# Optimization experiments

Hardware: AMD Instinct MI355X
Metric: run time of the kernel (lower is better)

## Reference

```python
import jax, jax.numpy as jnp
import numpy as np

LN_EPS = 1e-5  # torch nn.LayerNorm default


def _ln(x, g, b):
    m = x.mean(-1, keepdims=True)
    v = ((x - m) ** 2).mean(-1, keepdims=True)
    return (x - m) / jnp.sqrt(v + LN_EPS) * g + b


def setup_inputs() -> dict:
    key = jax.random.key(0)
    ks = jax.random.split(key, 4)
    N, S, D, C = 64, 512, 512, 1024
    return {
        "sequence": jax.random.normal(ks[0], (N, S, D), dtype=jnp.float32),
        "input_mask": jnp.ones((N, S), dtype=jnp.float32),
        "START": jnp.zeros((D,), dtype=jnp.float32),
        "W_init": (jax.random.normal(ks[1], (D, D), dtype=jnp.float32) / np.sqrt(D)).astype(jnp.float32),
        "b_init": jnp.zeros((D,), dtype=jnp.float32),
        "W1": (jax.random.normal(ks[2], (2 * D, C), dtype=jnp.float32) / np.sqrt(2 * D)).astype(jnp.float32),
        "b1": jnp.zeros((C,), dtype=jnp.float32),
        "W2": (jax.random.normal(ks[3], (C, 4 * D), dtype=jnp.float32) / np.sqrt(C)).astype(jnp.float32),
        "b2": jnp.zeros((4 * D,), dtype=jnp.float32),
        "ln_g": jnp.ones((D,), dtype=jnp.float32),
        "ln_b": jnp.zeros((D,), dtype=jnp.float32),
    }


def reference(sequence, input_mask, START, W_init, b_init, W1, b1, W2, b2, ln_g, ln_b):
    N, S, D = sequence.shape
    mask = input_mask[..., None]                      # [N,S,1]
    seq = sequence * mask
    # initial transform: LN(Linear(x)), then re-mask
    seq = _ln(seq @ W_init + b_init, ln_g, ln_b) * mask

    ht0 = jnp.broadcast_to(START, (N, D))

    def step(carry, xs):
        ht, gs = carry
        x, m = xs                                     # x: [N,D], m: [N,1]
        cat = jnp.concatenate([ht, x], axis=-1)       # [N,2D]
        inter = jax.nn.gelu(cat @ W1 + b1)            # [N,C] (dropout: eval mode)
        contents = (inter @ W2 + b2).reshape(N, 4, D)
        gates = jax.nn.sigmoid(contents[:, :3])       # f1, f2, i
        f1, f2, i = gates[:, 0], gates[:, 1], gates[:, 2]
        parent = contents[:, 3]
        ht_new = _ln(f1 * ht + f2 * x + i * parent, ln_g, ln_b)
        gs_new = m * ht_new + (1.0 - m) * gs
        return (ht_new, gs_new), ht_new

    xs = (jnp.swapaxes(seq, 0, 1), jnp.swapaxes(mask, 0, 1))  # time-major
    (ht, global_state), outs = jax.lax.scan(step, (ht0, ht0), xs)
    out_seq = jnp.swapaxes(outs, 0, 1) * mask         # [N,S,D]
    return out_seq, global_state
```

## Files before the change

kernel.cpp:

```cpp
#include <hip/hip_runtime.h>
#include <math.h>

#define DD 512
#define SS 512
#define NB 64
#define CC 1024
#define FF 2048
#define LN_EPS 1e-5f

__device__ __forceinline__ float sigf(float x) {
  return 1.0f / (1.0f + __expf(-x));
}
__device__ __forceinline__ float geluf(float x) {
  float u = 1.5957691216057308f * (x + 0.044715f * x * x * x);
  return x / (1.0f + __expf(-u));
}

__device__ __forceinline__ float cload(const float* p) {
  return __hip_atomic_load(p, __ATOMIC_RELAXED, __HIP_MEMORY_SCOPE_AGENT);
}
__device__ __forceinline__ unsigned cloadu(const unsigned* p) {
  return __hip_atomic_load(p, __ATOMIC_RELAXED, __HIP_MEMORY_SCOPE_AGENT);
}
__device__ __forceinline__ unsigned long long cload8(
    const unsigned long long* p) {
  return __hip_atomic_load(p, __ATOMIC_RELAXED, __HIP_MEMORY_SCOPE_AGENT);
}
__device__ __forceinline__ void cstore(float* p, float v) {
  __hip_atomic_store(p, v, __ATOMIC_RELAXED, __HIP_MEMORY_SCOPE_AGENT);
}
__device__ __forceinline__ void cstoreu(unsigned* p, unsigned v) {
  __hip_atomic_store(p, v, __ATOMIC_RELAXED, __HIP_MEMORY_SCOPE_AGENT);
}
__device__ __forceinline__ void cstore2(float* p, float a, float b) {
  float2 v = make_float2(a, b);
  unsigned long long u;
  __builtin_memcpy(&u, &v, 8);
  __hip_atomic_store((unsigned long long*)p, u, __ATOMIC_RELAXED,
                     __HIP_MEMORY_SCOPE_AGENT);
}
__device__ __forceinline__ float2 u2f2(unsigned long long u) {
  float2 f;
  __builtin_memcpy(&f, &u, 8);
  return f;
}

__device__ __forceinline__ void gbar(unsigned* __restrict__ flags,
                                     unsigned ep) {
  asm volatile("s_waitcnt vmcnt(0) lgkmcnt(0)" ::: "memory");
  __syncthreads();
  if (threadIdx.x < 64) {
    if (threadIdx.x == 0) cstoreu(&flags[blockIdx.x], ep);
    const unsigned* fp = flags + (threadIdx.x << 2);
    for (;;) {
      unsigned f0 = cloadu(fp + 0);
      unsigned f1 = cloadu(fp + 1);
      unsigned f2 = cloadu(fp + 2);
      unsigned f3 = cloadu(fp + 3);
      int ok = (f0 >= ep) & (f1 >= ep) & (f2 >= ep) & (f3 >= ep);
      if (__all(ok)) break;
      __builtin_amdgcn_s_sleep(1);
    }
  }
  __syncthreads();
}

__global__ __launch_bounds__(256) void k_gemm_init(
    const float* __restrict__ A, const float* __restrict__ mask,
    const float* __restrict__ W, const float* __restrict__ bias,
    float* __restrict__ out) {
  __shared__ float As[16][65];
  __shared__ float Bs[16][65];
  const int tid = threadIdx.x;
  const int bm = blockIdx.y * 64;
  const int bn = blockIdx.x * 64;
  const int tx = tid & 15;
  const int ty = tid >> 4;
  const int idx = tid * 4;
  const int am = idx >> 4;
  const int ak = idx & 15;
  const int bk = idx >> 6;
  const int bn2 = idx & 63;
  const float mrow = mask[bm + am];
  float acc[4][4] = {};
  for (int k0 = 0; k0 < DD; k0 += 16) {
    float4 av = *(const float4*)(A + (size_t)(bm + am) * DD + k0 + ak);
    As[ak + 0][am] = av.x * mrow;
    As[ak + 1][am] = av.y * mrow;
    As[ak + 2][am] = av.z * mrow;
    As[ak + 3][am] = av.w * mrow;
    float4 bv = *(const float4*)(W + (size_t)(k0 + bk) * DD + bn + bn2);
    Bs[bk][bn2 + 0] = bv.x;
    Bs[bk][bn2 + 1] = bv.y;
    Bs[bk][bn2 + 2] = bv.z;
    Bs[bk][bn2 + 3] = bv.w;
    __syncthreads();
#pragma unroll
    for (int kk = 0; kk < 16; ++kk) {
      float a0 = As[kk][ty * 4 + 0], a1 = As[kk][ty * 4 + 1];
      float a2 = As[kk][ty * 4 + 2], a3 = As[kk][ty * 4 + 3];
      float b0 = Bs[kk][tx * 4 + 0], b1v = Bs[kk][tx * 4 + 1];
      float b2v = Bs[kk][tx * 4 + 2], b3 = Bs[kk][tx * 4 + 3];
      acc[0][0] = fmaf(a0, b0, acc[0][0]);
      acc[0][1] = fmaf(a0, b1v, acc[0][1]);
      acc[0][2] = fmaf(a0, b2v, acc[0][2]);
      acc[0][3] = fmaf(a0, b3, acc[0][3]);
      acc[1][0] = fmaf(a1, b0, acc[1][0]);
      acc[1][1] = fmaf(a1, b1v, acc[1][1]);
      acc[1][2] = fmaf(a1, b2v, acc[1][2]);
      acc[1][3] = fmaf(a1, b3, acc[1][3]);
      acc[2][0] = fmaf(a2, b0, acc[2][0]);
      acc[2][1] = fmaf(a2, b1v, acc[2][1]);
      acc[2][2] = fmaf(a2, b2v, acc[2][2]);
      acc[2][3] = fmaf(a2, b3, acc[2][3]);
      acc[3][0] = fmaf(a3, b0, acc[3][0]);
      acc[3][1] = fmaf(a3, b1v, acc[3][1]);
      acc[3][2] = fmaf(a3, b2v, acc[3][2]);
      acc[3][3] = fmaf(a3, b3, acc[3][3]);
    }
    __syncthreads();
  }
#pragma unroll
  for (int i2 = 0; i2 < 4; ++i2) {
    int row = bm + ty * 4 + i2;
#pragma unroll
    for (int j = 0; j < 4; ++j) {
      int col = bn + tx * 4 + j;
      out[(size_t)row * DD + col] = acc[i2][j] + bias[col];
    }
  }
}

__global__ __launch_bounds__(256) void k_ln_rows(
    float* __restrict__ io, const float* __restrict__ mask,
    const float* __restrict__ g, const float* __restrict__ b) {
  const int r = blockIdx.x;
  float* row = io + (size_t)r * DD;
  const int tid = threadIdx.x;
  float x0 = row[tid], x1 = row[tid + 256];
  float s = x0 + x1, ss = x0 * x0 + x1 * x1;
#pragma unroll
  for (int off = 32; off > 0; off >>= 1) {
    s += __shfl_down(s, off, 64);
    ss += __shfl_down(ss, off, 64);
  }
  __shared__ float red[8];
  int lane = tid & 63, wv = tid >> 6;
  if (lane == 0) { red[wv] = s; red[4 + wv] = ss; }
  __syncthreads();
  s = red[0] + red[1] + red[2] + red[3];
  ss = red[4] + red[5] + red[6] + red[7];
  float mean = s * (1.0f / DD);
  float var = ss * (1.0f / DD) - mean * mean;
  float rs = rsqrtf(var + LN_EPS);
  float m = mask[r];
  row[tid] = ((x0 - mean) * rs * g[tid] + b[tid]) * m;
  row[tid + 256] = ((x1 - mean) * rs * g[tid + 256] + b[tid + 256]) * m;
}

__global__ __launch_bounds__(256) void k_xt(const float* __restrict__ seq2,
                                            float* __restrict__ xT) {
  __shared__ float tl[64][65];
  const int t = blockIdx.x;
  const int kt = blockIdx.y * 64;
  const int n = threadIdx.x >> 2;
  const int f = threadIdx.x & 3;
#pragma unroll
  for (int u = 0; u < 4; ++u) {
    int k = f * 16 + u * 4;
    float4 v = *(const float4*)(seq2 + ((size_t)n * SS + t) * DD + kt + k);
    tl[k + 0][n] = v.x;
    tl[k + 1][n] = v.y;
    tl[k + 2][n] = v.z;
    tl[k + 3][n] = v.w;
  }
  __syncthreads();
  const int k2 = threadIdx.x >> 2;
#pragma unroll
  for (int u = 0; u < 4; ++u) {
    int nn = f * 16 + u * 4;
    float4 v = make_float4(tl[k2][nn], tl[k2][nn + 1], tl[k2][nn + 2],
                           tl[k2][nn + 3]);
    *(float4*)(xT + ((size_t)t * DD + kt + k2) * 64 + nn) = v;
  }
}

__global__ __launch_bounds__(256) void k_pack1(const float* __restrict__ W1,
                                               const float* __restrict__ ln_g,
                                               float* __restrict__ W1p) {
  int i = blockIdx.x * 256 + threadIdx.x;
  int bcol = i >> 13;
  int k = (i >> 3) & 1023;
  int c = i & 7;
  float v = W1[(size_t)k * CC + (bcol << 3) + c];
  if (k < 512) v *= ln_g[k];
  W1p[i] = v;
}

__global__ __launch_bounds__(256) void k_pack2(const float* __restrict__ W2,
                                               float* __restrict__ W2p) {
  int i = blockIdx.x * 256 + threadIdx.x;
  int bcol = i >> 14;
  int k = (i >> 4) & 1023;
  int j = i & 15;
  int q = j & 3;
  int dd = j >> 2;
  W2p[i] = W2[(size_t)k * FF + q * 512 + (bcol << 2) + dd];
}

__global__ __launch_bounds__(128) void k_cols(
    const float* __restrict__ W1, const float* __restrict__ b1,
    const float* __restrict__ ln_g, const float* __restrict__ ln_b,
    const float* __restrict__ START, float* __restrict__ Qc,
    float* __restrict__ Blnc, float* __restrict__ H0c,
    unsigned* __restrict__ sync) {
  int c = blockIdx.x * 128 + threadIdx.x;
  sync[c] = 0u;
  float q = 0.f, bl = 0.f, h = 0.f;
  for (int k = 0; k < 512; ++k) {
    float wv = W1[(size_t)k * CC + c];
    q = fmaf(ln_g[k], wv, q);
    bl = fmaf(ln_b[k], wv, bl);
    h = fmaf(START[k], wv, h);
  }
  float bias = b1[c];
  Qc[c] = q;
  Blnc[c] = bl + bias;
  H0c[c] = h + bias;
}

__global__ __launch_bounds__(512, 1) void scan_kernel(
    float* __restrict__ outseq, float* __restrict__ gsout,
    const float* __restrict__ mask, const float* __restrict__ START,
    const float* __restrict__ W1p, const float* __restrict__ W2p,
    const float* __restrict__ b2, const float* __restrict__ ln_g,
    const float* __restrict__ ln_b, const float* __restrict__ Qc,
    const float* __restrict__ Blnc, const float* __restrict__ H0c,
    float* __restrict__ interT, float* __restrict__ zT,
    float* __restrict__ st_sum, float* __restrict__ st_ss,
    const float* __restrict__ xT, unsigned* __restrict__ sync,
    const int use_xt) {
  const int b = blockIdx.x;
  const int bcol = b >> 1;
  const int bhalf = b & 1;
  const int tid = threadIdx.x;
  const int w = tid >> 6;
  const int lane = tid & 63;
  unsigned ep = 0;

  __shared__ float4 pA4[8][64];
  __shared__ float4 pB4[8][64][2];
  __shared__ float W1s[8192];
  __shared__ float W2s[16384];

  {
    const float4* w1src = (const float4*)(W1p + ((size_t)bcol << 13));
    const float4* w2src = (const float4*)(W2p + ((size_t)bcol << 14));
#pragma unroll
    for (int i = 0; i < 4; ++i)
      ((float4*)W1s)[tid + 512 * i] = w1src[tid + 512 * i];
#pragma unroll
    for (int i = 0; i < 8; ++i)
      ((float4*)W2s)[tid + 512 * i] = w2src[tid + 512 * i];
  }

  const int on = (bhalf << 5) + (tid & 31);
  const int oh = tid >> 5;
  const int dbase = (bcol << 2) + (oh << 1);
  const int colbase = (bcol << 3) + (oh << 2);
  float ht0 = 0, ht1 = 0, gs0 = 0, gs1 = 0, z0 = 0, z1 = 0;
  float gg0 = 0, gg1 = 0, bb0 = 0, bb1 = 0, mn = 0, rv = 0;
  float4 Q4 = make_float4(0, 0, 0, 0), Bl4 = Q4, H04 = Q4;
  float bb2[8];
  if (tid < 64) {
    ht0 = START[dbase];
    ht1 = START[dbase + 1];
    gs0 = ht0;
    gs1 = ht1;
    gg0 = ln_g[dbase];
    gg1 = ln_g[dbase + 1];
    bb0 = ln_b[dbase];
    bb1 = ln_b[dbase + 1];
    Q4 = *(const float4*)(Qc + colbase);
    Bl4 = *(const float4*)(Blnc + colbase);
    H04 = *(const float4*)(H0c + colbase);
#pragma unroll
    for (int q = 0; q < 4; ++q) {
      bb2[q] = b2[q * 512 + dbase];
      bb2[4 + q] = b2[q * 512 + dbase + 1];
    }
  }
  __syncthreads();

  for (int t = 0; t < SS; ++t) {
    if (t > 0 && tid < 64) {
      const int par9 = ((t - 1) & 1) << 9;
      const float* sp = st_sum + par9 + (on << 3);
      const float* qp = st_ss + par9 + (on << 3);
      float s = 0.f, ss = 0.f;
#pragma unroll
      for (int i = 0; i < 8; ++i) {
        s += cload(sp + i);
        ss += cload(qp + i);
      }
      float mean = s * (1.0f / DD);
      float var = ss * (1.0f / DD) - mean * mean;
      float rsv = rsqrtf(var + LN_EPS);
      mn = mean;
      rv = rsv;
      float hn0 = (z0 - mean) * rsv * gg0 + bb0;
      float hn1 = (z1 - mean) * rsv * gg1 + bb1;
      float m = mask[on * SS + (t - 1)];
      float* op =
          outseq + (size_t)on * SS * DD + (size_t)(t - 1) * DD + dbase;
      if (use_xt) {
        *(float2*)op = make_float2(hn0 * m, hn1 * m);
      } else {
        cstore2(op, hn0 * m, hn1 * m);
      }
      gs0 = m * hn0 + (1.0f - m) * gs0;
      gs1 = m * hn1 + (1.0f - m) * gs1;
      ht0 = hn0;
      ht1 = hn1;
    }
    if (b == 0) {
      const int parz9 = (t & 1) << 9;
      cstore(st_sum + parz9 + tid, 0.f);
      cstore(st_ss + parz9 + tid, 0.f);
    }
    {
      const int h = lane >> 5;
      const int bl = lane & 31;
      float4 acc = make_float4(0.f, 0.f, 0.f, 0.f);
      if (w < 4) {
        if (t > 0) {
          const float* ap = zT + (w << 13) + (bhalf << 6) + (bl << 1);
          const float* wp = W1s + (w << 10);
          for (int c0 = 0; c0 < 64; c0 += 32) {
            unsigned long long v[32];
#pragma unroll
            for (int j = 0; j < 32; ++j)
              v[j] = cload8(
                  (const unsigned long long*)(ap + ((c0 + j) << 7)));
#pragma unroll
            for (int j = 0; j < 32; ++j) {
              float2 zv = u2f2(v[j]);
              const float* wr = wp + ((c0 + j) << 4) + (h << 2);
              acc.x = fmaf(zv.x, wr[0], acc.x);
              acc.y = fmaf(zv.x, wr[1], acc.y);
              acc.z = fmaf(zv.x, wr[2], acc.z);
              acc.w = fmaf(zv.x, wr[3], acc.w);
              acc.x = fmaf(zv.y, wr[8], acc.x);
              acc.y = fmaf(zv.y, wr[9], acc.y);
              acc.z = fmaf(zv.y, wr[10], acc.z);
              acc.w = fmaf(zv.y, wr[11], acc.w);
            }
          }
        }
      } else {
        const int kxb = (w - 4) << 7;
        const float* wp = W1s + ((512 + kxb) << 3);
        if (use_xt) {
          const float* xp =
              xT + (((size_t)t * DD + kxb) << 6) + (bhalf << 5) + bl;
          for (int c0 = 0; c0 < 128; c0 += 64) {
            float v[64];
#pragma unroll
            for (int j = 0; j < 64; ++j) v[j] = xp[(c0 + j) << 6];
#pragma unroll
            for (int j = 0; j < 64; ++j) {
              const float* wr = wp + ((c0 + j) << 3) + (h << 2);
              acc.x = fmaf(v[j], wr[0], acc.x);
              acc.y = fmaf(v[j], wr[1], acc.y);
              acc.z = fmaf(v[j], wr[2], acc.z);
              acc.w = fmaf(v[j], wr[3], acc.w);
            }
          }
        } else {
          const int n = (bhalf << 5) + bl;
          const float* op =
              outseq + (size_t)n * SS * DD + (size_t)t * DD + kxb;
          for (int c0 = 0; c0 < 128; c0 += 16) {
            float4 xv[4];
#pragma unroll
            for (int j = 0; j < 4; ++j)
              xv[j] = *(const float4*)(op + c0 + 4 * j);
#pragma unroll
            for (int j = 0; j < 16; ++j) {
              const float* wr = wp + ((c0 + j) << 3) + (h << 2);
              float x = ((const float*)xv)[j];
              acc.x = fmaf(x, wr[0], acc.x);
              acc.y = fmaf(x, wr[1], acc.y);
              acc.z = fmaf(x, wr[2], acc.z);
              acc.w = fmaf(x, wr[3], acc.w);
            }
          }
        }
      }
      pA4[w][lane] = acc;
    }
    __syncthreads();
    if (tid < 64) {
      float4 P = pA4[0][tid];
      float4 X = pA4[4][tid];
#pragma unroll
      for (int ww = 1; ww < 4; ++ww) {
        float4 p = pA4[ww][tid];
        P.x += p.x; P.y += p.y; P.z += p.z; P.w += p.w;
        float4 x4 = pA4[ww + 4][tid];
        X.x += x4.x; X.y += x4.y; X.z += x4.z; X.w += x4.w;
      }
      float4 o;
      if (t > 0) {
        float c1 = -rv * mn;
        o.x = fmaf(rv, P.x, fmaf(c1, Q4.x, Bl4.x)) + X.x;
        o.y = fmaf(rv, P.y, fmaf(c1, Q4.y, Bl4.y)) + X.y;
        o.z = fmaf(rv, P.z, fmaf(c1, Q4.z, Bl4.z)) + X.z;
        o.w = fmaf(rv, P.w, fmaf(c1, Q4.w, Bl4.w)) + X.w;
      } else {
        o.x = H04.x + X.x;
        o.y = H04.y + X.y;
        o.z = H04.z + X.z;
        o.w = H04.w + X.w;
      }
      cstore2(interT + ((colbase >> 1) << 7) + (on << 1), geluf(o.x),
              geluf(o.y));
      cstore2(interT + (((colbase >> 1) + 1) << 7) + (on << 1), geluf(o.z),
              geluf(o.w));
    }
    gbar(sync, ++ep);
    {
      const int h = lane >> 5;
      const int bl = lane & 31;
      float4 accL = make_float4(0.f, 0.f, 0.f, 0.f);
      float4 accH = make_float4(0.f, 0.f, 0.f, 0.f);
      const float* w2 = W2s + (w << 11);
      const float* ip = interT + (w << 13) + (bhalf << 6) + (bl << 1);
      for (int c0 = 0; c0 < 64; c0 += 32) {
        unsigned long long v[32];
#pragma unroll
        for (int j = 0; j < 32; ++j)
          v[j] = cload8((const unsigned long long*)(ip + ((c0 + j) << 7)));
#pragma unroll
        for (int j = 0; j < 32; ++j) {
          float2 iv = u2f2(v[j]);
          const float* wr = w2 + ((c0 + j) << 5) + (h << 3);
          accL.x = fmaf(iv.x, wr[0], accL.x);
          accL.y = fmaf(iv.x, wr[1], accL.y);
          accL.z = fmaf(iv.x, wr[2], accL.z);
          accL.w = fmaf(iv.x, wr[3], accL.w);
          accH.x = fmaf(iv.x, wr[4], accH.x);
          accH.y = fmaf(iv.x, wr[5], accH.y);
          accH.z = fmaf(iv.x, wr[6], accH.z);
          accH.w = fmaf(iv.x, wr[7], accH.w);
          accL.x = fmaf(iv.y, wr[16], accL.x);
          accL.y = fmaf(iv.y, wr[17], accL.y);
          accL.z = fmaf(iv.y, wr[18], accL.z);
          accL.w = fmaf(iv.y, wr[19], accL.w);
          accH.x = fmaf(iv.y, wr[20], accH.x);
          accH.y = fmaf(iv.y, wr[21], accH.y);
          accH.z = fmaf(iv.y, wr[22], accH.z);
          accH.w = fmaf(iv.y, wr[23], accH.w);
        }
      }
      pB4[w][lane][0] = accL;
      pB4[w][lane][1] = accH;
    }
    __syncthreads();
    if (tid < 64) {
      float4 lo = pB4[0][tid][0];
      float4 hi = pB4[0][tid][1];
#pragma unroll
      for (int ww = 1; ww < 8; ++ww) {
        float4 p = pB4[ww][tid][0];
        lo.x += p.x; lo.y += p.y; lo.z += p.z; lo.w += p.w;
        float4 q = pB4[ww][tid][1];
        hi.x += q.x; hi.y += q.y; hi.z += q.z; hi.w += q.w;
      }
      lo.x += bb2[0]; lo.y += bb2[1]; lo.z += bb2[2]; lo.w += bb2[3];
      hi.x += bb2[4]; hi.y += bb2[5]; hi.z += bb2[6]; hi.w += bb2[7];
      float x0, x1;
      if (use_xt) {
        x0 = xT[((size_t)t * DD + dbase) * 64 + on];
        x1 = xT[((size_t)t * DD + dbase + 1) * 64 + on];
      } else {
        float2 x2 = *(const float2*)(outseq + (size_t)on * SS * DD +
                                     (size_t)t * DD + dbase);
        x0 = x2.x;
        x1 = x2.y;
      }
      z0 = sigf(lo.x) * ht0 + sigf(lo.y) * x0 + sigf(lo.z) * lo.w;
      z1 = sigf(hi.x) * ht1 + sigf(hi.y) * x1 + sigf(hi.z) * hi.w;
      cstore2(zT + ((dbase >> 1) << 7) + (on << 1), z0, z1);
      const int par9 = (t & 1) << 9;
      const int slot = bcol & 7;
      atomicAdd(st_sum + par9 + (on << 3) + slot, z0 + z1);
      atomicAdd(st_ss + par9 + (on << 3) + slot, z0 * z0 + z1 * z1);
    }
    gbar(sync, ++ep);
  }
  if (tid < 64) {
    const int par9 = ((SS - 1) & 1) << 9;
    const float* sp = st_sum + par9 + (on << 3);
    const float* qp = st_ss + par9 + (on << 3);
    float s = 0.f, ss = 0.f;
#pragma unroll
    for (int i = 0; i < 8; ++i) {
      s += cload(sp + i);
      ss += cload(qp + i);
    }
    float mean = s * (1.0f / DD);
    float var = ss * (1.0f / DD) - mean * mean;
    float rsv = rsqrtf(var + LN_EPS);
    float hn0 = (z0 - mean) * rsv * gg0 + bb0;
    float hn1 = (z1 - mean) * rsv * gg1 + bb1;
    float m = mask[on * SS + (SS - 1)];
    *(float2*)(outseq + (size_t)on * SS * DD + (size_t)(SS - 1) * DD +
               dbase) = make_float2(hn0 * m, hn1 * m);
    gs0 = m * hn0 + (1.0f - m) * gs0;
    gs1 = m * hn1 + (1.0f - m) * gs1;
    *(float2*)(gsout + on * DD + dbase) = make_float2(gs0, gs1);
  }
}

extern "C" void kernel_launch(void* const* d_in, const int* in_sizes, int n_in,
                              void* d_out, int out_size, void* d_ws,
                              size_t ws_size, hipStream_t stream) {
  const float* seq = (const float*)d_in[0];
  const float* mask = (const float*)d_in[1];
  const float* START = (const float*)d_in[2];
  const float* W_init = (const float*)d_in[3];
  const float* b_init = (const float*)d_in[4];
  const float* W1 = (const float*)d_in[5];
  const float* b1 = (const float*)d_in[6];
  const float* W2 = (const float*)d_in[7];
  const float* b2 = (const float*)d_in[8];
  const float* ln_g = (const float*)d_in[9];
  const float* ln_b = (const float*)d_in[10];

  float* out = (float*)d_out;
  float* outseq = out;
  float* gsout = out + (size_t)NB * SS * DD;

  float* W1p = (float*)d_ws;
  float* W2p = W1p + 1048576;
  float* interT = W2p + 2097152;
  float* zT = interT + 65536;
  float* st_sum = zT + 32768;
  float* st_ss = st_sum + 4096;
  float* Qc = st_ss + 4096;
  float* Blnc = Qc + 1024;
  float* H0c = Blnc + 1024;
  unsigned* syncw = (unsigned*)(H0c + 1024);
  float* xT = (float*)(syncw + 1024);
  const size_t base_floats = 1048576 + 2097152 + 65536 + 32768 + 4096 + 4096 +
                             1024 + 1024 + 1024 + 1024;
  const int use_xt =
      (ws_size >= (base_floats + (size_t)16777216) * 4) ? 1 : 0;

  dim3 ga(DD / 64, (NB * SS) / 64);
  k_gemm_init<<<ga, 256, 0, stream>>>(seq, mask, W_init, b_init, outseq);
  k_ln_rows<<<NB * SS, 256, 0, stream>>>(outseq, mask, ln_g, ln_b);
  if (use_xt) {
    k_xt<<<dim3(SS, 8), 256, 0, stream>>>(outseq, xT);
  }
  k_pack1<<<4096, 256, 0, stream>>>(W1, ln_g, W1p);
  k_pack2<<<8192, 256, 0, stream>>>(W2, W2p);
  k_cols<<<8, 128, 0, stream>>>(W1, b1, ln_g, ln_b, START, Qc, Blnc, H0c,
                                syncw);

  scan_kernel<<<256, 512, 0, stream>>>(outseq, gsout, mask, START, W1p, W2p,
                                       b2, ln_g, ln_b, Qc, Blnc, H0c, interT,
                                       zT, st_sum, st_ss, xT, syncw, use_xt);
}
```

Before: 18.12 ms.

## Double scan block size to 1024 threads and software-pipeline partial-product loads

Raises the persistent scan kernel from 512 to 1024 threads per block, so each wave handles half as much of the K dimension in both GEMV phases, and shared partial-sum buffers grow to 16 slots. The inner loops are rewritten as double-buffered 8-element load/consume chains that interleave coherent global loads with FMAs. The aim is more latency hiding per step of the serial recurrence. In exchange, the cross-wave reductions get longer and register pressure under the 1024-thread launch bound is tighter.

```diff
diff --git a/kernel.cpp b/kernel.cpp
--- a/kernel.cpp
+++ b/kernel.cpp
@@ -8,6 +8,8 @@
 #define FF 2048
 #define LN_EPS 1e-5f
 
+typedef unsigned long long ull;
+
 __device__ __forceinline__ float sigf(float x) {
   return 1.0f / (1.0f + __expf(-x));
 }
@@ -22,8 +24,7 @@
 __device__ __forceinline__ unsigned cloadu(const unsigned* p) {
   return __hip_atomic_load(p, __ATOMIC_RELAXED, __HIP_MEMORY_SCOPE_AGENT);
 }
-__device__ __forceinline__ unsigned long long cload8(
-    const unsigned long long* p) {
+__device__ __forceinline__ ull cload8(const ull* p) {
   return __hip_atomic_load(p, __ATOMIC_RELAXED, __HIP_MEMORY_SCOPE_AGENT);
 }
 __device__ __forceinline__ void cstore(float* p, float v) {
@@ -34,12 +35,11 @@
 }
 __device__ __forceinline__ void cstore2(float* p, float a, float b) {
   float2 v = make_float2(a, b);
-  unsigned long long u;
+  ull u;
   __builtin_memcpy(&u, &v, 8);
-  __hip_atomic_store((unsigned long long*)p, u, __ATOMIC_RELAXED,
-                     __HIP_MEMORY_SCOPE_AGENT);
-}
-__device__ __forceinline__ float2 u2f2(unsigned long long u) {
+  __hip_atomic_store((ull*)p, u, __ATOMIC_RELAXED, __HIP_MEMORY_SCOPE_AGENT);
+}
+__device__ __forceinline__ float2 u2f2(ull u) {
   float2 f;
   __builtin_memcpy(&f, &u, 8);
   return f;
@@ -229,7 +229,61 @@
   H0c[c] = h + bias;
 }
 
-__global__ __launch_bounds__(512, 1) void scan_kernel(
+#define ZCONS(V, CB)                                        \
+  _Pragma("unroll") for (int j = 0; j < 8; ++j) {           \
+    float2 zv = u2f2(V[j]);                                 \
+    const float* wr = wp + (((CB) + j) << 4);               \
+    acc.x = fmaf(zv.x, wr[0], acc.x);                       \
+    acc.y = fmaf(zv.x, wr[1], acc.y);                       \
+    acc.z = fmaf(zv.x, wr[2], acc.z);                       \
+    acc.w = fmaf(zv.x, wr[3], acc.w);                       \
+    acc.x = fmaf(zv.y, wr[8], acc.x);                       \
+    acc.y = fmaf(zv.y, wr[9], acc.y);                       \
+    acc.z = fmaf(zv.y, wr[10], acc.z);                      \
+    acc.w = fmaf(zv.y, wr[11], acc.w);                      \
+  }
+#define ZLOAD(V, CB)                                        \
+  _Pragma("unroll") for (int j = 0; j < 8; ++j)             \
+      V[j] = cload8((const ull*)(ap + (((CB) + j) << 7)));
+
+#define XCONS(V, CB)                                        \
+  _Pragma("unroll") for (int j = 0; j < 8; ++j) {           \
+    const float* wr = wp + (((CB) + j) << 3);               \
+    acc.x = fmaf(V[j], wr[0], acc.x);                       \
+    acc.y = fmaf(V[j], wr[1], acc.y);                       \
+    acc.z = fmaf(V[j], wr[2], acc.z);                       \
+    acc.w = fmaf(V[j], wr[3], acc.w);                       \
+  }
+#define XLOAD(V, CB)                                        \
+  _Pragma("unroll") for (int j = 0; j < 8; ++j)             \
+      V[j] = xp[(((CB) + j)) << 6];
+
+#define BCONS(V, CB)                                        \
+  _Pragma("unroll") for (int j = 0; j < 8; ++j) {           \
+    float2 iv = u2f2(V[j]);                                 \
+    const float* wr = w2 + (((CB) + j) << 5);               \
+    accL.x = fmaf(iv.x, wr[0], accL.x);                     \
+    accL.y = fmaf(iv.x, wr[1], accL.y);                     \
+    accL.z = fmaf(iv.x, wr[2], accL.z);                     \
+    accL.w = fmaf(iv.x, wr[3], accL.w);                     \
+    accH.x = fmaf(iv.x, wr[4], accH.x);                     \
+    accH.y = fmaf(iv.x, wr[5], accH.y);                     \
+    accH.z = fmaf(iv.x, wr[6], accH.z);                     \
+    accH.w = fmaf(iv.x, wr[7], accH.w);                     \
+    accL.x = fmaf(iv.y, wr[16], accL.x);                    \
+    accL.y = fmaf(iv.y, wr[17], accL.y);                    \
+    accL.z = fmaf(iv.y, wr[18], accL.z);                    \
+    accL.w = fmaf(iv.y, wr[19], accL.w);                    \
+    accH.x = fmaf(iv.y, wr[20], accH.x);                    \
+    accH.y = fmaf(iv.y, wr[21], accH.y);                    \
+    accH.z = fmaf(iv.y, wr[22], accH.z);                    \
+    accH.w = fmaf(iv.y, wr[23], accH.w);                    \
+  }
+#define BLOAD(V, CB)                                        \
+  _Pragma("unroll") for (int j = 0; j < 8; ++j)             \
+      V[j] = cload8((const ull*)(ip + (((CB) + j) << 7)));
+
+__global__ __launch_bounds__(1024, 4) void scan_kernel(
     float* __restrict__ outseq, float* __restrict__ gsout,
     const float* __restrict__ mask, const float* __restrict__ START,
     const float* __restrict__ W1p, const float* __restrict__ W2p,
@@ -248,8 +302,8 @@
   const int lane = tid & 63;
   unsigned ep = 0;
 
-  __shared__ float4 pA4[8][64];
-  __shared__ float4 pB4[8][64][2];
+  __shared__ float4 pA4[16][64];
+  __shared__ float4 pB4[16][64][2];
   __shared__ float W1s[8192];
   __shared__ float W2s[16384];
 
@@ -257,11 +311,11 @@
     const float4* w1src = (const float4*)(W1p + ((size_t)bcol << 13));
     const float4* w2src = (const float4*)(W2p + ((size_t)bcol << 14));
 #pragma unroll
+    for (int i = 0; i < 2; ++i)
+      ((float4*)W1s)[tid + 1024 * i] = w1src[tid + 1024 * i];
+#pragma unroll
     for (int i = 0; i < 4; ++i)
-      ((float4*)W1s)[tid + 512 * i] = w1src[tid + 512 * i];
-#pragma unroll
-    for (int i = 0; i < 8; ++i)
-      ((float4*)W2s)[tid + 512 * i] = w2src[tid + 512 * i];
+      ((float4*)W2s)[tid + 1024 * i] = w2src[tid + 1024 * i];
   }
 
   const int on = (bhalf << 5) + (tid & 31);
@@ -323,7 +377,7 @@
       ht0 = hn0;
       ht1 = hn1;
     }
-    if (b == 0) {
+    if (b == 0 && tid < 512) {
       const int parz9 = (t & 1) << 9;
       cstore(st_sum + parz9 + tid, 0.f);
       cstore(st_ss + parz9 + tid, 0.f);
@@ -332,62 +386,52 @@
       const int h = lane >> 5;
       const int bl = lane & 31;
       float4 acc = make_float4(0.f, 0.f, 0.f, 0.f);
-      if (w < 4) {
+      if (w < 8) {
         if (t > 0) {
-          const float* ap = zT + (w << 13) + (bhalf << 6) + (bl << 1);
-          const float* wp = W1s + (w << 10);
-          for (int c0 = 0; c0 < 64; c0 += 32) {
-            unsigned long long v[32];
-#pragma unroll
-            for (int j = 0; j < 32; ++j)
-              v[j] = cload8(
-                  (const unsigned long long*)(ap + ((c0 + j) << 7)));
-#pragma unroll
-            for (int j = 0; j < 32; ++j) {
-              float2 zv = u2f2(v[j]);
-              const float* wr = wp + ((c0 + j) << 4) + (h << 2);
-              acc.x = fmaf(zv.x, wr[0], acc.x);
-              acc.y = fmaf(zv.x, wr[1], acc.y);
-              acc.z = fmaf(zv.x, wr[2], acc.z);
-              acc.w = fmaf(zv.x, wr[3], acc.w);
-              acc.x = fmaf(zv.y, wr[8], acc.x);
-              acc.y = fmaf(zv.y, wr[9], acc.y);
-              acc.z = fmaf(zv.y, wr[10], acc.z);
-              acc.w = fmaf(zv.y, wr[11], acc.w);
-            }
-          }
+          const int kpb = w << 5;
+          const float* ap = zT + (kpb << 7) + (bhalf << 6) + (bl << 1);
+          const float* wp = W1s + (kpb << 4) + (h << 2);
+          ull v0[8], v1[8];
+          ZLOAD(v0, 0)
+          ZLOAD(v1, 8)
+          ZCONS(v0, 0)
+          ZLOAD(v0, 16)
+          ZCONS(v1, 8)
+          ZLOAD(v1, 24)
+          ZCONS(v0, 16)
+          ZCONS(v1, 24)
         }
       } else {
-        const int kxb = (w - 4) << 7;
-        const float* wp = W1s + ((512 + kxb) << 3);
+        const int kxb = (w - 8) << 6;
         if (use_xt) {
           const float* xp =
               xT + (((size_t)t * DD + kxb) << 6) + (bhalf << 5) + bl;
-          for (int c0 = 0; c0 < 128; c0 += 64) {
-            float v[64];
-#pragma unroll
-            for (int j = 0; j < 64; ++j) v[j] = xp[(c0 + j) << 6];
-#pragma unroll
-            for (int j = 0; j < 64; ++j) {
-              const float* wr = wp + ((c0 + j) << 3) + (h << 2);
-              acc.x = fmaf(v[j], wr[0], acc.x);
-              acc.y = fmaf(v[j], wr[1], acc.y);
-              acc.z = fmaf(v[j], wr[2], acc.z);
-              acc.w = fmaf(v[j], wr[3], acc.w);
-            }
+          const float* wp = W1s + ((512 + kxb) << 3) + (h << 2);
+          float v0[8], v1[8];
+          XLOAD(v0, 0)
+          XLOAD(v1, 8)
+#pragma unroll
+          for (int c0 = 0; c0 < 48; c0 += 16) {
+            XCONS(v0, c0)
+            XLOAD(v0, c0 + 16)
+            XCONS(v1, c0 + 8)
+            XLOAD(v1, c0 + 24)
           }
+          XCONS(v0, 48)
+          XCONS(v1, 56)
         } else {
           const int n = (bhalf << 5) + bl;
           const float* op =
               outseq + (size_t)n * SS * DD + (size_t)t * DD + kxb;
-          for (int c0 = 0; c0 < 128; c0 += 16) {
+          const float* wp = W1s + ((512 + kxb) << 3) + (h << 2);
+          for (int c0 = 0; c0 < 64; c0 += 16) {
             float4 xv[4];
 #pragma unroll
             for (int j = 0; j < 4; ++j)
               xv[j] = *(const float4*)(op + c0 + 4 * j);
 #pragma unroll
             for (int j = 0; j < 16; ++j) {
-              const float* wr = wp + ((c0 + j) << 3) + (h << 2);
+              const float* wr = wp + ((c0 + j) << 3);
               float x = ((const float*)xv)[j];
               acc.x = fmaf(x, wr[0], acc.x);
               acc.y = fmaf(x, wr[1], acc.y);
@@ -402,12 +446,15 @@
     __syncthreads();
     if (tid < 64) {
       float4 P = pA4[0][tid];
-      float4 X = pA4[4][tid];
-#pragma unroll
-      for (int ww = 1; ww < 4; ++ww) {
+#pragma unroll
+      for (int ww = 1; ww < 8; ++ww) {
         float4 p = pA4[ww][tid];
         P.x += p.x; P.y += p.y; P.z += p.z; P.w += p.w;
-        float4 x4 = pA4[ww + 4][tid];
+      }
+      float4 X = pA4[8][tid];
+#pragma unroll
+      for (int ww = 9; ww < 16; ++ww) {
+        float4 x4 = pA4[ww][tid];
         X.x += x4.x; X.y += x4.y; X.z += x4.z; X.w += x4.w;
       }
       float4 o;
@@ -434,35 +481,18 @@
       const int bl = lane & 31;
       float4 accL = make_float4(0.f, 0.f, 0.f, 0.f);
       float4 accH = make_float4(0.f, 0.f, 0.f, 0.f);
-      const float* w2 = W2s + (w << 11);
-      const float* ip = interT + (w << 13) + (bhalf << 6) + (bl << 1);
-      for (int c0 = 0; c0 < 64; c0 += 32) {
-        unsigned long long v[32];
-#pragma unroll
-        for (int j = 0; j < 32; ++j)
-          v[j] = cload8((const unsigned long long*)(ip + ((c0 + j) << 7)));
-#pragma unroll
-        for (int j = 0; j < 32; ++j) {
-          float2 iv = u2f2(v[j]);
-          const float* wr = w2 + ((c0 + j) << 5) + (h << 3);
-          accL.x = fmaf(iv.x, wr[0], accL.x);
-          accL.y = fmaf(iv.x, wr[1], accL.y);
-          accL.z = fmaf(iv.x, wr[2], accL.z);
-          accL.w = fmaf(iv.x, wr[3], accL.w);
-          accH.x = fmaf(iv.x, wr[4], accH.x);
-          accH.y = fmaf(iv.x, wr[5], accH.y);
-          accH.z = fmaf(iv.x, wr[6], accH.z);
-          accH.w = fmaf(iv.x, wr[7], accH.w);
-          accL.x = fmaf(iv.y, wr[16], accL.x);
-          accL.y = fmaf(iv.y, wr[17], accL.y);
-          accL.z = fmaf(iv.y, wr[18], accL.z);
-          accL.w = fmaf(iv.y, wr[19], accL.w);
-          accH.x = fmaf(iv.y, wr[20], accH.x);
-          accH.y = fmaf(iv.y, wr[21], accH.y);
-          accH.z = fmaf(iv.y, wr[22], accH.z);
-          accH.w = fmaf(iv.y, wr[23], accH.w);
-        }
-      }
+      const int kpb = w << 5;
+      const float* w2 = W2s + (kpb << 5) + (h << 3);
+      const float* ip = interT + (kpb << 7) + (bhalf << 6) + (bl << 1);
+      ull v0[8], v1[8];
+      BLOAD(v0, 0)
+      BLOAD(v1, 8)
+      BCONS(v0, 0)
+      BLOAD(v0, 16)
+      BCONS(v1, 8)
+      BLOAD(v1, 24)
+      BCONS(v0, 16)
+      BCONS(v1, 24)
       pB4[w][lane][0] = accL;
       pB4[w][lane][1] = accH;
     }
@@ -471,7 +501,7 @@
       float4 lo = pB4[0][tid][0];
       float4 hi = pB4[0][tid][1];
 #pragma unroll
-      for (int ww = 1; ww < 8; ++ww) {
+      for (int ww = 1; ww < 16; ++ww) {
         float4 p = pB4[ww][tid][0];
         lo.x += p.x; lo.y += p.y; lo.z += p.z; lo.w += p.w;
         float4 q = pB4[ww][tid][1];
@@ -569,7 +599,7 @@
   k_cols<<<8, 128, 0, stream>>>(W1, b1, ln_g, ln_b, START, Qc, Blnc, H0c,
                                 syncw);
 
-  scan_kernel<<<256, 512, 0, stream>>>(outseq, gsout, mask, START, W1p, W2p,
-                                       b2, ln_g, ln_b, Qc, Blnc, H0c, interT,
-                                       zT, st_sum, st_ss, xT, syncw, use_xt);
-}
+  scan_kernel<<<256, 1024, 0, stream>>>(outseq, gsout, mask, START, W1p, W2p,
+                                        b2, ln_g, ln_b, Qc, Blnc, H0c, interT,
+                                        zT, st_sum, st_ss, xT, syncw, use_xt);
+}
```

After: 21.58 ms. 19.1% more time.
